# Performance work log

Hardware: AMD Instinct MI355X
Metric: run time of the kernel (lower is better)

The kernel has to match this reference:

```python
import jax, jax.numpy as jnp
import numpy as np

NEG_SLOPE = 0.2  # PyG GATConv default negative_slope


def gat_conv(x, src, dst, W, a_src, a_dst, b, concat):
    """One PyG-style GATConv (with self-loops already in src/dst).
    x: [N, F_in], W: [F_in, H*C], a_src/a_dst: [H, C], b: [H*C] or [C].
    """
    N = x.shape[0]
    H, C = a_src.shape
    h = (x @ W).reshape(N, H, C)                      # [N,H,C]
    al_s = jnp.einsum('nhc,hc->nh', h, a_src)         # [N,H]
    al_d = jnp.einsum('nhc,hc->nh', h, a_dst)
    e = al_s[src] + al_d[dst]                         # [E,H]
    e = jnp.where(e >= 0, e, NEG_SLOPE * e)           # leaky_relu
    # softmax over edges grouped by destination node
    emax = jax.ops.segment_max(e, dst, num_segments=N)  # [N,H]
    ex = jnp.exp(e - emax[dst])
    denom = jax.ops.segment_sum(ex, dst, num_segments=N)
    alpha = ex / denom[dst]                           # [E,H]
    msg = h[src] * alpha[:, :, None]                  # [E,H,C]
    out = jax.ops.segment_sum(msg, dst, num_segments=N)  # [N,H,C]
    out = out.reshape(N, H * C) if concat else out.mean(axis=1)
    return out + b


def setup_inputs() -> dict:
    key = jax.random.key(0)
    ks = jax.random.split(key, 10)
    N, E = 100000, 1600000
    F_in, Hc, H, F_out = 128, 64, 2, 64
    x = jax.random.normal(ks[0], (N, F_in), dtype=jnp.float32)
    edge_index = jax.random.randint(ks[1], (2, E), 0, N, dtype=jnp.int64)
    s1 = 1.0 / np.sqrt(F_in)
    W1 = jax.random.uniform(ks[2], (F_in, H * Hc), jnp.float32, -s1, s1)
    a_src1 = jax.random.normal(ks[3], (H, Hc), jnp.float32) * 0.1
    a_dst1 = jax.random.normal(ks[4], (H, Hc), jnp.float32) * 0.1
    b1 = jnp.zeros((H * Hc,), jnp.float32)
    s2 = 1.0 / np.sqrt(H * Hc)
    W2 = jax.random.uniform(ks[5], (H * Hc, H * F_out), jnp.float32, -s2, s2)
    a_src2 = jax.random.normal(ks[6], (H, F_out), jnp.float32) * 0.1
    a_dst2 = jax.random.normal(ks[7], (H, F_out), jnp.float32) * 0.1
    b2 = jnp.zeros((F_out,), jnp.float32)
    return {"x": x, "edge_index": edge_index,
            "W1": W1, "a_src1": a_src1, "a_dst1": a_dst1, "b1": b1,
            "W2": W2, "a_src2": a_src2, "a_dst2": a_dst2, "b2": b2}


def reference(x, edge_index, W1, a_src1, a_dst1, b1, W2, a_src2, a_dst2, b2):
    N = x.shape[0]
    loops = jnp.arange(N, dtype=edge_index.dtype)
    src = jnp.concatenate([edge_index[0], loops])  # PyG GATConv adds self-loops
    dst = jnp.concatenate([edge_index[1], loops])
    h = gat_conv(x, src, dst, W1, a_src1, a_dst1, b1, concat=True)
    h = jax.nn.elu(h)
    out = gat_conv(h, src, dst, W2, a_src2, a_dst2, b2, concat=False)
    return out
```

## Files before the change

### kernel.cpp

```cpp
#include <hip/hip_runtime.h>
#include <hip/hip_fp16.h>

#define NEG_SLOPE 0.2f

__device__ inline unsigned enc_max(float f) {
    unsigned b = __float_as_uint(f);
    return (b & 0x80000000u) ? ~b : (b | 0x80000000u);
}
__device__ inline float dec_max(unsigned k) {
    return (k & 0x80000000u) ? __uint_as_float(k ^ 0x80000000u)
                             : __uint_as_float(~k);
}

__device__ inline void row_out(int r, int N, int lane, float A0, float A1,
                               float as0, float as1, float ad0, float ad1,
                               __half* __restrict__ H16, float* __restrict__ AL,
                               float& rmax)
{
    if (r >= N) return;
    ((__half2*)H16)[(size_t)r * 64 + lane] = __float22half2_rn(make_float2(A0, A1));
    float ps = A0 * as0 + A1 * as1;
    float pd = A0 * ad0 + A1 * ad1;
#pragma unroll
    for (int off = 16; off > 0; off >>= 1) {
        ps += __shfl_xor(ps, off, 64);
        pd += __shfl_xor(pd, off, 64);
    }
    rmax = fmaxf(rmax, ps);
    if (lane == 0)       { AL[(size_t)r * 4 + 0] = ps; AL[(size_t)r * 4 + 2] = pd; }
    else if (lane == 32) { AL[(size_t)r * 4 + 1] = ps; AL[(size_t)r * 4 + 3] = pd; }
}

__global__ __launch_bounds__(512) void gemm_al_kernel(
    const float* __restrict__ X, const float* __restrict__ W,
    const float* __restrict__ asrc, const float* __restrict__ adst,
    __half* __restrict__ H16, float* __restrict__ AL,
    unsigned* __restrict__ ubp, int N)
{
    __shared__ alignas(16) __half Wh[32 * 64 * 8];
    __shared__ float xb[8][4][128];

    const int t = threadIdx.x, lane = t & 63, wave = t >> 6;

    {
        const float2* Wg = (const float2*)W;
#pragma unroll
        for (int idx = t; idx < 2048; idx += 512) {
            const int kq = idx >> 6, l = idx & 63;
            __half2* dst = (__half2*)&Wh[(size_t)(kq * 64 + l) * 8];
#pragma unroll
            for (int i = 0; i < 4; i++) {
                float2 w = Wg[(4 * kq + i) * 64 + l];
                dst[i] = __float22half2_rn(w);
            }
        }
    }
    __syncthreads();

    const float as0 = asrc[2 * lane], as1 = asrc[2 * lane + 1];
    const float ad0 = adst[2 * lane], ad1 = adst[2 * lane + 1];

    const int i0 = lane, i1 = lane + 64;
    const int r0i = i0 >> 5, k0i = i0 & 31;
    const int r1i = i1 >> 5, k1i = i1 & 31;
    const int rowbase = (blockIdx.x * 8 + wave) * 16;
    float rmax = -__builtin_inff();

    float4 pA = make_float4(0, 0, 0, 0), pB = make_float4(0, 0, 0, 0);
    if (rowbase + r0i < N) pA = ((const float4*)(X + (size_t)(rowbase + r0i) * 128))[k0i];
    if (rowbase + r1i < N) pB = ((const float4*)(X + (size_t)(rowbase + r1i) * 128))[k1i];

    for (int c = 0; c < 4; c++) {
        const int rbase = rowbase + c * 4;
        if (rbase >= N) break;

        ((float4*)xb[wave][r0i])[k0i] = pA;
        ((float4*)xb[wave][r1i])[k1i] = pB;

        if (c < 3) {
            const int nb = rowbase + (c + 1) * 4;
            pA = make_float4(0, 0, 0, 0); pB = make_float4(0, 0, 0, 0);
            if (nb + r0i < N) pA = ((const float4*)(X + (size_t)(nb + r0i) * 128))[k0i];
            if (nb + r1i < N) pB = ((const float4*)(X + (size_t)(nb + r1i) * 128))[k1i];
        }

        float2 acc[4];
#pragma unroll
        for (int r = 0; r < 4; r++) acc[r] = make_float2(0.f, 0.f);

#pragma unroll 4
        for (int kq = 0; kq < 32; kq++) {
            const uint4 wraw = ((const uint4*)Wh)[kq * 64 + lane];
            const __half2* wh = (const __half2*)&wraw;
            const float2 w0 = __half22float2(wh[0]);
            const float2 w1 = __half22float2(wh[1]);
            const float2 w2 = __half22float2(wh[2]);
            const float2 w3 = __half22float2(wh[3]);
#pragma unroll
            for (int r = 0; r < 4; r++) {
                const float4 xr = ((const float4*)xb[wave][r])[kq];
                acc[r].x = fmaf(xr.x, w0.x, acc[r].x);
                acc[r].y = fmaf(xr.x, w0.y, acc[r].y);
                acc[r].x = fmaf(xr.y, w1.x, acc[r].x);
                acc[r].y = fmaf(xr.y, w1.y, acc[r].y);
                acc[r].x = fmaf(xr.z, w2.x, acc[r].x);
                acc[r].y = fmaf(xr.z, w2.y, acc[r].y);
                acc[r].x = fmaf(xr.w, w3.x, acc[r].x);
                acc[r].y = fmaf(xr.w, w3.y, acc[r].y);
            }
        }
#pragma unroll
        for (int r = 0; r < 4; r++)
            row_out(rbase + r, N, lane, acc[r].x, acc[r].y,
                    as0, as1, ad0, ad1, H16, AL, rmax);
    }

    __syncthreads();
    float* red = (float*)xb;
    if (lane == 0)       red[wave * 2 + 0] = rmax;
    else if (lane == 32) red[wave * 2 + 1] = rmax;
    __syncthreads();
    if (t < 2) {
        float m = red[t];
#pragma unroll
        for (int i = 1; i < 8; i++) m = fmaxf(m, red[2 * i + t]);
        atomicMax(&ubp[t], enc_max(m));
    }
}

__global__ void count_kernel(const int* __restrict__ edst, int* __restrict__ cnt,
                             int E, int N)
{
    int i = blockIdx.x * 256 + threadIdx.x;
    if (i < E)            atomicAdd(&cnt[edst[i]], 1);
    else if (i < E + N)   atomicAdd(&cnt[i - E], 1);
}

__global__ void scan_local_kernel(const int* __restrict__ in, int* __restrict__ out,
                                  int* __restrict__ bsum, int n)
{
    __shared__ int sm[1024];
    const int t = threadIdx.x;
    const int i = blockIdx.x * 1024 + t;
    int v = (i < n) ? in[i] : 0;
    sm[t] = v;
    __syncthreads();
    for (int off = 1; off < 1024; off <<= 1) {
        int x = (t >= off) ? sm[t - off] : 0;
        __syncthreads();
        sm[t] += x;
        __syncthreads();
    }
    if (i < n) out[i] = sm[t];
    if (t == 1023) bsum[blockIdx.x] = sm[t];
}

__global__ void scan_excl_single_kernel(int* __restrict__ a, int B)
{
    __shared__ int sm[1024];
    const int t = threadIdx.x;
    int v = (t < B) ? a[t] : 0;
    sm[t] = v;
    __syncthreads();
    for (int off = 1; off < 1024; off <<= 1) {
        int x = (t >= off) ? sm[t - off] : 0;
        __syncthreads();
        sm[t] += x;
        __syncthreads();
    }
    if (t < B) a[t] = sm[t] - v;
}

__global__ void finalize_csr_kernel(const int* __restrict__ incl,
                                    const int* __restrict__ cnt,
                                    const int* __restrict__ bexcl,
                                    int* __restrict__ dstptr, int* __restrict__ cursor,
                                    int N, int Etot)
{
    const int i = blockIdx.x * 1024 + threadIdx.x;
    if (i < N) {
        int v = incl[i] + bexcl[i >> 10] - cnt[i];
        dstptr[i] = v;
        cursor[i] = v;
    }
    if (i == N) dstptr[N] = Etot;
}

__global__ void scatter_kernel(const int* __restrict__ esrc, const int* __restrict__ edst,
                               int* __restrict__ cursor, int* __restrict__ ssrc,
                               int E, int N, int sliceN, int bps)
{
    const int slice = blockIdx.x & 7;
    const int dlo = slice * sliceN;
    const int dhi = min(N, dlo + sliceN);
    const int Etot = E + N;
    for (int i = (blockIdx.x >> 3) * 256 + (int)threadIdx.x; i < Etot; i += bps * 256) {
        int s, d;
        if (i < E) { s = esrc[i]; d = edst[i]; }
        else       { s = d = i - E; }
        if (d >= dlo && d < dhi) {
            int pos = atomicAdd(&cursor[d], 1);
            ssrc[pos] = s;
        }
    }
}

__global__ __launch_bounds__(256) void aggregate_kernel(
    const __half* __restrict__ H16, const float* __restrict__ AL,
    const int* __restrict__ dstptr, const int* __restrict__ ssrc,
    const unsigned* __restrict__ ubenc, const float* __restrict__ bias,
    float* __restrict__ out, int N, int mode)
{
    const int wid  = (blockIdx.x * blockDim.x + threadIdx.x) >> 6;
    const int lane = threadIdx.x & 63;
    if (wid * 2 >= N) return;
    const int nl   = lane & 31;
    const int n    = wid * 2 + (lane >> 5);
    const bool act = (n < N);
    const int nn   = act ? n : (N - 1);
    const int beg  = dstptr[nn];
    const int end  = act ? dstptr[nn + 1] : beg;

    const int head = nl >> 4;
    const float ald = AL[(size_t)nn * 4 + 2 + head];
    float ub = dec_max(ubenc[head]) + ald;
    ub = (ub >= 0.f) ? ub : NEG_SLOPE * ub;

    const int nblk = (end - beg + 3) >> 2;
    const int trips = max(nblk, __shfl_xor(nblk, 32, 64));

    float s = 0.f, a0 = 0.f, a1 = 0.f, a2 = 0.f, a3 = 0.f;

    int sA[4];
    float e0[4], e1[4];
    uint2 g0[4], g1[4];

    auto LSRC = [&](int b, int (&sv)[4]) {
#pragma unroll
        for (int k = 0; k < 4; k++) {
            const int idx = beg + 4 * b + k;
            const int v = ssrc[idx];
            sv[k] = (idx < end) ? v : -1;
        }
    };
    auto LHE = [&](const int (&sv)[4], float (&e)[4], uint2 (&g)[4]) {
#pragma unroll
        for (int k = 0; k < 4; k++) {
            const int src = (sv[k] >= 0) ? sv[k] : 0;
            const float a = AL[(size_t)src * 4 + head];
            e[k] = (sv[k] >= 0) ? a : -__builtin_inff();
            g[k] = ((const uint2*)(H16 + (size_t)src * 128))[nl];
        }
    };

    {
        int ta[4], tb[4];
        LSRC(0, ta); LSRC(1, tb); LSRC(2, sA);
        LHE(ta, e0, g0);
        LHE(tb, e1, g1);
    }

    for (int t = 0; t < trips; t++) {
        int sB[4];
        LSRC(t + 3, sB);
        float e2[4]; uint2 g2[4];
        LHE(sA, e2, g2);
#pragma unroll
        for (int k = 0; k < 4; k++) {
            float tt = e0[k] + ald;
            tt = (tt >= 0.f) ? tt : NEG_SLOPE * tt;
            const float p = __expf(tt - ub);
            s += p;
            const __half2* ph = (const __half2*)&g0[k];
            const float2 f01 = __half22float2(ph[0]);
            const float2 f23 = __half22float2(ph[1]);
            a0 = fmaf(p, f01.x, a0);
            a1 = fmaf(p, f01.y, a1);
            a2 = fmaf(p, f23.x, a2);
            a3 = fmaf(p, f23.y, a3);
        }
#pragma unroll
        for (int k = 0; k < 4; k++) {
            e0[k] = e1[k]; g0[k] = g1[k];
            e1[k] = e2[k]; g1[k] = g2[k];
            sA[k] = sB[k];
        }
    }

    if (!act) return;
    const float inv = 1.f / s;
    float o0 = a0 * inv, o1 = a1 * inv, o2 = a2 * inv, o3 = a3 * inv;

    if (mode == 0) {
        const float4 b4 = ((const float4*)bias)[nl];
        o0 += b4.x; o1 += b4.y; o2 += b4.z; o3 += b4.w;
        o0 = (o0 > 0.f) ? o0 : (__expf(o0) - 1.f);
        o1 = (o1 > 0.f) ? o1 : (__expf(o1) - 1.f);
        o2 = (o2 > 0.f) ? o2 : (__expf(o2) - 1.f);
        o3 = (o3 > 0.f) ? o3 : (__expf(o3) - 1.f);
        ((float4*)out)[(size_t)n * 32 + nl] = make_float4(o0, o1, o2, o3);
    } else {
        const float q0 = __shfl_xor(o0, 16, 64);
        const float q1 = __shfl_xor(o1, 16, 64);
        const float q2 = __shfl_xor(o2, 16, 64);
        const float q3 = __shfl_xor(o3, 16, 64);
        if (nl < 16) {
            const float4 b4 = ((const float4*)bias)[nl];
            ((float4*)out)[(size_t)n * 16 + nl] =
                make_float4(0.5f * (o0 + q0) + b4.x, 0.5f * (o1 + q1) + b4.y,
                            0.5f * (o2 + q2) + b4.z, 0.5f * (o3 + q3) + b4.w);
        }
    }
}

extern "C" void kernel_launch(void* const* d_in, const int* in_sizes, int n_in,
                              void* d_out, int out_size, void* d_ws, size_t ws_size,
                              hipStream_t stream)
{
    const float* x   = (const float*)d_in[0];
    const int*   eix = (const int*)d_in[1];
    const float* W1  = (const float*)d_in[2];
    const float* as1 = (const float*)d_in[3];
    const float* ad1 = (const float*)d_in[4];
    const float* b1  = (const float*)d_in[5];
    const float* W2  = (const float*)d_in[6];
    const float* as2 = (const float*)d_in[7];
    const float* ad2 = (const float*)d_in[8];
    const float* b2  = (const float*)d_in[9];
    float* out = (float*)d_out;

    const int N = in_sizes[0] / 128;
    const int E = in_sizes[1] / 2;
    const int Etot = E + N;
    const int* esrc = eix;
    const int* edst = eix + E;

    char* p = (char*)d_ws;
    __half*   h16    = (__half*)p;   p += (size_t)N * 128 * 2;
    float*    y1     = (float*)p;    p += (size_t)N * 128 * 4;
    float*    al     = (float*)p;    p += (size_t)N * 4 * 4;
    int*      cnt    = (int*)p;      p += (size_t)N * 4;
    unsigned* ub     = (unsigned*)p; p += 64;
    int*      incl   = (int*)p;      p += (size_t)N * 4;
    int*      dstptr = (int*)p;      p += (size_t)(N + 1) * 4;
    int*      cursor = (int*)p;      p += (size_t)N * 4;
    int*      bs1    = (int*)p;      p += 1024 * 4;
    int*      ssrc   = (int*)p;      p += (size_t)(Etot + 256) * 4;

    hipMemsetAsync(cnt, 0, (size_t)N * 4 + 64, stream);

    {
        const int eblocks = (Etot + 255) / 256;
        const int B0 = (N + 1023) / 1024;
        count_kernel<<<eblocks, 256, 0, stream>>>(edst, cnt, E, N);
        scan_local_kernel<<<B0, 1024, 0, stream>>>(cnt, incl, bs1, N);
        scan_excl_single_kernel<<<1, 1024, 0, stream>>>(bs1, B0);
        finalize_csr_kernel<<<(N + 1024) / 1024, 1024, 0, stream>>>(
            incl, cnt, bs1, dstptr, cursor, N, Etot);
        const int sliceN = (N + 7) / 8;
        const int bps = 512;
        scatter_kernel<<<bps * 8, 256, 0, stream>>>(esrc, edst, cursor, ssrc,
                                                    E, N, sliceN, bps);
    }

    const int ggrid = (N + 127) / 128;
    const int nwaves = (N + 1) / 2;
    const int ablocks = (nwaves + 3) / 4;

    gemm_al_kernel<<<ggrid, 512, 0, stream>>>(x, W1, as1, ad1, h16, al, ub, N);
    aggregate_kernel<<<ablocks, 256, 0, stream>>>(h16, al, dstptr, ssrc, ub, b1, y1, N, 0);

    gemm_al_kernel<<<ggrid, 512, 0, stream>>>(y1, W2, as2, ad2, h16, al, ub + 2, N);
    aggregate_kernel<<<ablocks, 256, 0, stream>>>(h16, al, dstptr, ssrc, ub + 2, b2, out, N, 1);
}
```

Before: 459.5 us.

## Use MFMA f16 matrix instructions for the feature GEMM with swizzled LDS

Replaces the scalar FMA GEMM in gemm_al_kernel with 16x16x16 f16 MFMA instructions. X and W are converted to half and staged in XOR-swizzled shared memory, and each block now handles 64 rows with 256 threads. Attention logits are reduced from the accumulator layout via shuffles, and the output is staged through LDS for coalesced half stores. X is now rounded to f16 before the multiply, which costs some input precision. The GEMM is only one part of the pipeline alongside the aggregation and CSR-build kernels.

Result: faster. 377.0 us (-18.0%).

```diff
diff --git a/kernel.cpp b/kernel.cpp
--- a/kernel.cpp
+++ b/kernel.cpp
@@ -2,6 +2,10 @@
 #include <hip/hip_fp16.h>
 
 #define NEG_SLOPE 0.2f
+
+typedef _Float16 half4v __attribute__((ext_vector_type(4)));
+typedef _Float16 half8v __attribute__((ext_vector_type(8)));
+typedef float f32x4 __attribute__((ext_vector_type(4)));
 
 __device__ inline unsigned enc_max(float f) {
     unsigned b = __float_as_uint(f);
@@ -12,119 +16,139 @@
                              : __uint_as_float(~k);
 }
 
-__device__ inline void row_out(int r, int N, int lane, float A0, float A1,
-                               float as0, float as1, float ad0, float ad1,
-                               __half* __restrict__ H16, float* __restrict__ AL,
-                               float& rmax)
-{
-    if (r >= N) return;
-    ((__half2*)H16)[(size_t)r * 64 + lane] = __float22half2_rn(make_float2(A0, A1));
-    float ps = A0 * as0 + A1 * as1;
-    float pd = A0 * ad0 + A1 * ad1;
-#pragma unroll
-    for (int off = 16; off > 0; off >>= 1) {
-        ps += __shfl_xor(ps, off, 64);
-        pd += __shfl_xor(pd, off, 64);
-    }
-    rmax = fmaxf(rmax, ps);
-    if (lane == 0)       { AL[(size_t)r * 4 + 0] = ps; AL[(size_t)r * 4 + 2] = pd; }
-    else if (lane == 32) { AL[(size_t)r * 4 + 1] = ps; AL[(size_t)r * 4 + 3] = pd; }
-}
-
-__global__ __launch_bounds__(512) void gemm_al_kernel(
+__global__ __launch_bounds__(256) void gemm_al_kernel(
     const float* __restrict__ X, const float* __restrict__ W,
     const float* __restrict__ asrc, const float* __restrict__ adst,
     __half* __restrict__ H16, float* __restrict__ AL,
     unsigned* __restrict__ ubp, int N)
 {
-    __shared__ alignas(16) __half Wh[32 * 64 * 8];
-    __shared__ float xb[8][4][128];
+    __shared__ alignas(16) char smem[49152];
 
     const int t = threadIdx.x, lane = t & 63, wave = t >> 6;
-
+    const int r0 = blockIdx.x * 64;
+
+#pragma unroll
+    for (int i = 0; i < 8; i++) {
+        const int f = t + i * 256;
+        const int row = f >> 5, k4 = f & 31;
+        const int k8 = k4 >> 1, hf = k4 & 1;
+        float4 v = make_float4(0.f, 0.f, 0.f, 0.f);
+        if (r0 + row < N) v = ((const float4*)X)[(size_t)(r0 + row) * 32 + k4];
+        half4v h = { (_Float16)v.x, (_Float16)v.y, (_Float16)v.z, (_Float16)v.w };
+        const int slot = row * 16 + (k8 ^ (row & 7));
+        *(half4v*)(smem + slot * 16 + hf * 8) = h;
+    }
     {
-        const float2* Wg = (const float2*)W;
-#pragma unroll
-        for (int idx = t; idx < 2048; idx += 512) {
-            const int kq = idx >> 6, l = idx & 63;
-            __half2* dst = (__half2*)&Wh[(size_t)(kq * 64 + l) * 8];
-#pragma unroll
-            for (int i = 0; i < 4; i++) {
-                float2 w = Wg[(4 * kq + i) * 64 + l];
-                dst[i] = __float22half2_rn(w);
+        const int c = t >> 1, kh = t & 1;
+        const float* Wc = W + c;
+#pragma unroll
+        for (int i8 = 0; i8 < 8; i8++) {
+            const int k0 = kh * 64 + i8 * 8;
+            half8v h;
+#pragma unroll
+            for (int j = 0; j < 8; j++) h[j] = (_Float16)Wc[(size_t)(k0 + j) * 128];
+            const int slot = c * 16 + ((k0 >> 3) ^ (c & 7));
+            *(half8v*)(smem + 16384 + slot * 16) = h;
+        }
+    }
+    __syncthreads();
+
+    const int mrow = wave * 16 + (lane & 15);
+    const int kg = lane >> 4;
+    half4v a[8];
+#pragma unroll
+    for (int ks = 0; ks < 8; ks++) {
+        const int k0 = ks * 16 + kg * 4;
+        const int slot = mrow * 16 + ((k0 >> 3) ^ (mrow & 7));
+        a[ks] = *(const half4v*)(smem + slot * 16 + (k0 & 7) * 2);
+    }
+    f32x4 acc[8];
+#pragma unroll
+    for (int ct = 0; ct < 8; ct++) acc[ct] = (f32x4){0.f, 0.f, 0.f, 0.f};
+#pragma unroll
+    for (int ct = 0; ct < 8; ct++) {
+        const int c = ct * 16 + (lane & 15);
+        const char* sbase = smem + 16384 + c * 256;
+        const int csw = c & 7;
+#pragma unroll
+        for (int ks = 0; ks < 8; ks++) {
+            const int k0 = ks * 16 + kg * 4;
+            const int slot = (k0 >> 3) ^ csw;
+            half4v b = *(const half4v*)(sbase + slot * 16 + (k0 & 7) * 2);
+            acc[ct] = __builtin_amdgcn_mfma_f32_16x16x16f16(a[ks], b, acc[ct], 0, 0, 0);
+        }
+    }
+
+    float psh0[4] = {0,0,0,0}, psh1[4] = {0,0,0,0};
+    float pdh0[4] = {0,0,0,0}, pdh1[4] = {0,0,0,0};
+#pragma unroll
+    for (int ct = 0; ct < 8; ct++) {
+        const int c = ct * 16 + (lane & 15);
+        const float as = asrc[c], ad = adst[c];
+#pragma unroll
+        for (int r = 0; r < 4; r++) {
+            if (ct < 4) { psh0[r] = fmaf(acc[ct][r], as, psh0[r]);
+                          pdh0[r] = fmaf(acc[ct][r], ad, pdh0[r]); }
+            else        { psh1[r] = fmaf(acc[ct][r], as, psh1[r]);
+                          pdh1[r] = fmaf(acc[ct][r], ad, pdh1[r]); }
+        }
+    }
+#pragma unroll
+    for (int off = 1; off <= 8; off <<= 1) {
+#pragma unroll
+        for (int r = 0; r < 4; r++) {
+            psh0[r] += __shfl_xor(psh0[r], off, 64);
+            psh1[r] += __shfl_xor(psh1[r], off, 64);
+            pdh0[r] += __shfl_xor(pdh0[r], off, 64);
+            pdh1[r] += __shfl_xor(pdh1[r], off, 64);
+        }
+    }
+    float rmax0 = -__builtin_inff(), rmax1 = -__builtin_inff();
+    if ((lane & 15) == 0) {
+#pragma unroll
+        for (int r = 0; r < 4; r++) {
+            const int gr = r0 + wave * 16 + (lane >> 4) * 4 + r;
+            if (gr < N) {
+                ((float4*)AL)[gr] = make_float4(psh0[r], psh1[r], pdh0[r], pdh1[r]);
+                rmax0 = fmaxf(rmax0, psh0[r]);
+                rmax1 = fmaxf(rmax1, psh1[r]);
             }
         }
     }
-    __syncthreads();
-
-    const float as0 = asrc[2 * lane], as1 = asrc[2 * lane + 1];
-    const float ad0 = adst[2 * lane], ad1 = adst[2 * lane + 1];
-
-    const int i0 = lane, i1 = lane + 64;
-    const int r0i = i0 >> 5, k0i = i0 & 31;
-    const int r1i = i1 >> 5, k1i = i1 & 31;
-    const int rowbase = (blockIdx.x * 8 + wave) * 16;
-    float rmax = -__builtin_inff();
-
-    float4 pA = make_float4(0, 0, 0, 0), pB = make_float4(0, 0, 0, 0);
-    if (rowbase + r0i < N) pA = ((const float4*)(X + (size_t)(rowbase + r0i) * 128))[k0i];
-    if (rowbase + r1i < N) pB = ((const float4*)(X + (size_t)(rowbase + r1i) * 128))[k1i];
-
-    for (int c = 0; c < 4; c++) {
-        const int rbase = rowbase + c * 4;
-        if (rbase >= N) break;
-
-        ((float4*)xb[wave][r0i])[k0i] = pA;
-        ((float4*)xb[wave][r1i])[k1i] = pB;
-
-        if (c < 3) {
-            const int nb = rowbase + (c + 1) * 4;
-            pA = make_float4(0, 0, 0, 0); pB = make_float4(0, 0, 0, 0);
-            if (nb + r0i < N) pA = ((const float4*)(X + (size_t)(nb + r0i) * 128))[k0i];
-            if (nb + r1i < N) pB = ((const float4*)(X + (size_t)(nb + r1i) * 128))[k1i];
-        }
-
-        float2 acc[4];
-#pragma unroll
-        for (int r = 0; r < 4; r++) acc[r] = make_float2(0.f, 0.f);
-
-#pragma unroll 4
-        for (int kq = 0; kq < 32; kq++) {
-            const uint4 wraw = ((const uint4*)Wh)[kq * 64 + lane];
-            const __half2* wh = (const __half2*)&wraw;
-            const float2 w0 = __half22float2(wh[0]);
-            const float2 w1 = __half22float2(wh[1]);
-            const float2 w2 = __half22float2(wh[2]);
-            const float2 w3 = __half22float2(wh[3]);
-#pragma unroll
-            for (int r = 0; r < 4; r++) {
-                const float4 xr = ((const float4*)xb[wave][r])[kq];
-                acc[r].x = fmaf(xr.x, w0.x, acc[r].x);
-                acc[r].y = fmaf(xr.x, w0.y, acc[r].y);
-                acc[r].x = fmaf(xr.y, w1.x, acc[r].x);
-                acc[r].y = fmaf(xr.y, w1.y, acc[r].y);
-                acc[r].x = fmaf(xr.z, w2.x, acc[r].x);
-                acc[r].y = fmaf(xr.z, w2.y, acc[r].y);
-                acc[r].x = fmaf(xr.w, w3.x, acc[r].x);
-                acc[r].y = fmaf(xr.w, w3.y, acc[r].y);
-            }
-        }
-#pragma unroll
-        for (int r = 0; r < 4; r++)
-            row_out(rbase + r, N, lane, acc[r].x, acc[r].y,
-                    as0, as1, ad0, ad1, H16, AL, rmax);
-    }
-
-    __syncthreads();
-    float* red = (float*)xb;
-    if (lane == 0)       red[wave * 2 + 0] = rmax;
-    else if (lane == 32) red[wave * 2 + 1] = rmax;
+#pragma unroll
+    for (int off = 32; off > 0; off >>= 1) {
+        rmax0 = fmaxf(rmax0, __shfl_xor(rmax0, off, 64));
+        rmax1 = fmaxf(rmax1, __shfl_xor(rmax1, off, 64));
+    }
+
+    __syncthreads();
+    float* Dst = (float*)smem;
+    float* red = (float*)(smem + 33792);
+    if (lane == 0) { red[wave * 2] = rmax0; red[wave * 2 + 1] = rmax1; }
+#pragma unroll
+    for (int ct = 0; ct < 8; ct++) {
+        const int col = ct * 16 + (lane & 15);
+        float* drow = Dst + wave * 2112 + ((lane >> 4) * 4) * 132 + col;
+#pragma unroll
+        for (int r = 0; r < 4; r++) drow[r * 132] = acc[ct][r];
+    }
     __syncthreads();
     if (t < 2) {
-        float m = red[t];
-#pragma unroll
-        for (int i = 1; i < 8; i++) m = fmaxf(m, red[2 * i + t]);
+        float m = fmaxf(fmaxf(red[t], red[2 + t]), fmaxf(red[4 + t], red[6 + t]));
         atomicMax(&ubp[t], enc_max(m));
+    }
+#pragma unroll
+    for (int i = 0; i < 4; i++) {
+        const int f = t + i * 256;
+        const int row = f >> 4, c16 = f & 15;
+        if (r0 + row < N) {
+            const float* src = Dst + (row >> 4) * 2112 + (row & 15) * 132 + c16 * 8;
+            const float4 v0 = *(const float4*)src;
+            const float4 v1 = *(const float4*)(src + 4);
+            half8v h = { (_Float16)v0.x, (_Float16)v0.y, (_Float16)v0.z, (_Float16)v0.w,
+                         (_Float16)v1.x, (_Float16)v1.y, (_Float16)v1.z, (_Float16)v1.w };
+            *(half8v*)((_Float16*)H16 + (size_t)(r0 + row) * 128 + c16 * 8) = h;
+        }
     }
 }
 
@@ -363,13 +387,13 @@
                                                     E, N, sliceN, bps);
     }
 
-    const int ggrid = (N + 127) / 128;
+    const int ggrid = (N + 63) / 64;
     const int nwaves = (N + 1) / 2;
     const int ablocks = (nwaves + 3) / 4;
 
-    gemm_al_kernel<<<ggrid, 512, 0, stream>>>(x, W1, as1, ad1, h16, al, ub, N);
+    gemm_al_kernel<<<ggrid, 256, 0, stream>>>(x, W1, as1, ad1, h16, al, ub, N);
     aggregate_kernel<<<ablocks, 256, 0, stream>>>(h16, al, dstptr, ssrc, ub, b1, y1, N, 0);
 
-    gemm_al_kernel<<<ggrid, 512, 0, stream>>>(y1, W2, as2, ad2, h16, al, ub + 2, N);
+    gemm_al_kernel<<<ggrid, 256, 0, stream>>>(y1, W2, as2, ad2, h16, al, ub + 2, N);
     aggregate_kernel<<<ablocks, 256, 0, stream>>>(h16, al, dstptr, ssrc, ub + 2, b2, out, N, 1);
 }
```
